# Kernel optimization log

Hardware: AMD Instinct MI355X
Metric: run time of the kernel (lower is better)

## Reference

```python
import jax, jax.numpy as jnp
import numpy as np

K_DIM, V_DIM, D_K, D_V, N_HEAD = 1024, 1024, 64, 64, 16


def setup_inputs() -> dict:
    key = jax.random.key(0)
    ks = jax.random.split(key, 7)
    B, LQ, LK = 2, 2048, 2048
    q = jax.random.normal(ks[0], (B, LQ, K_DIM), dtype=jnp.float32)
    k = jax.random.normal(ks[1], (B, LK, K_DIM), dtype=jnp.float32)
    v = jax.random.normal(ks[2], (B, LK, V_DIM), dtype=jnp.float32)
    s = 0.02
    w_q = jax.random.normal(ks[3], (N_HEAD * D_K, K_DIM), dtype=jnp.float32) * s
    w_k = jax.random.normal(ks[4], (N_HEAD * D_K, K_DIM), dtype=jnp.float32) * s
    w_v = jax.random.normal(ks[5], (N_HEAD * D_V, V_DIM), dtype=jnp.float32) * s
    fc_y = jax.random.normal(ks[6], (V_DIM, N_HEAD * D_V), dtype=jnp.float32) * s
    return {"q": q, "k": k, "v": v, "w_q": w_q, "w_k": w_k, "w_v": w_v, "fc_y": fc_y}


def reference(q, k, v, w_q, w_k, w_v, fc_y):
    B, LQ, _ = q.shape
    LK = k.shape[1]
    # projections: Linear(x) = x @ W.T, then split heads -> (b, h, l, d)
    qh = (q @ w_q.T).reshape(B, LQ, N_HEAD, D_K).transpose(0, 2, 1, 3)
    kh = (k @ w_k.T).reshape(B, LK, N_HEAD, D_K).transpose(0, 2, 1, 3)
    vh = (v @ w_v.T).reshape(B, LK, N_HEAD, D_V).transpose(0, 2, 1, 3)
    # NOTE: original ScaledDotProductAttention uses k.size(2), which for
    # 4D (b, h, len_k, d_k) inputs is len_k, NOT d_k. Replicate faithfully.
    scale = kh.shape[2] ** 0.5  # == sqrt(len_k)
    scores = jnp.einsum('bhqd,bhkd->bhqk', qh, kh) / scale
    attn = jax.nn.softmax(scores, axis=-1)  # (b, h, lq, lk)
    yh = jnp.einsum('bhqk,bhkd->bhqd', attn, vh)
    y = yh.transpose(0, 2, 1, 3).reshape(B, LQ, N_HEAD * D_V)
    y = y @ fc_y.T  # (b, lq, v_dim)
    return (y, attn)
```

## Files before the change

### kernel.cpp

```cpp
#include <hip/hip_runtime.h>

typedef __attribute__((ext_vector_type(8))) short short8;
typedef __attribute__((ext_vector_type(4))) short short4v;
typedef __attribute__((ext_vector_type(4))) float f32x4;

__device__ __forceinline__ short f2bf(float f) {
  unsigned u = __float_as_uint(f);
  u += 0x7fff + ((u >> 16) & 1);
  return (short)(u >> 16);
}

__device__ __forceinline__ void async16(const short* g, short* l) {
  __builtin_amdgcn_global_load_lds(
      (__attribute__((address_space(1))) unsigned int*)(g),
      (__attribute__((address_space(3))) unsigned int*)(l), 16, 0, 0);
}

__global__ __launch_bounds__(256) void cvt_w(const float* __restrict__ w0, const float* __restrict__ w1,
                                             const float* __restrict__ w2, const float* __restrict__ w3,
                                             short* __restrict__ o0, short* __restrict__ o1,
                                             short* __restrict__ o2, short* __restrict__ o3) {
  const int bid = blockIdx.x;
  const int seg = bid >> 9;
  const float* s = seg == 0 ? w0 : seg == 1 ? w1 : seg == 2 ? w2 : w3;
  short* d = seg == 0 ? o0 : seg == 1 ? o1 : seg == 2 ? o2 : o3;
  const int idx = ((bid & 511) * 256 + (int)threadIdx.x) * 8;
  float4 x = *(const float4*)(s + idx);
  float4 y = *(const float4*)(s + idx + 4);
  short8 t;
  t[0] = f2bf(x.x); t[1] = f2bf(x.y); t[2] = f2bf(x.z); t[3] = f2bf(x.w);
  t[4] = f2bf(y.x); t[5] = f2bf(y.y); t[6] = f2bf(y.z); t[7] = f2bf(y.w);
  *(short8*)(d + idx) = t;
}

__device__ __forceinline__ void ldf32(const float* src, int K, int kt, int tid, f32x4* r) {
  const int row = tid >> 4, c = (tid & 15) * 4;
  const float* p = src + (long)row * K + kt + c;
#pragma unroll
  for (int j = 0; j < 8; j++) r[j] = *(const f32x4*)(p + (long)(j * 16) * K);
}
__device__ __forceinline__ void wrf32(short* dst, int stride, int tid, const f32x4* r) {
  const int row = tid >> 4, c = (tid & 15) * 4;
#pragma unroll
  for (int j = 0; j < 8; j++) {
    short4v t;
    t[0] = f2bf(r[j][0]); t[1] = f2bf(r[j][1]); t[2] = f2bf(r[j][2]); t[3] = f2bf(r[j][3]);
    *(short4v*)&dst[(row + j * 16) * stride + c] = t;
  }
}
__device__ __forceinline__ void ldbf16(const short* src, int K, int kt, int tid, short* lds) {
  const int w = tid >> 6, l = tid & 63;
#pragma unroll
  for (int i = 0; i < 4; i++) {
    const int seg = i * 4 + w;
    const int o = seg * 1024 + l * 16;
    const int row = o >> 7, col = (o & 127) >> 1;
    async16(src + (long)row * K + kt + col, lds + seg * 512);
  }
}

template <int AF32, int BF32, int MODE>
__device__ __forceinline__ void gemm_core(const void* Ap, const void* Bp, void* Cout,
                                          int bm, int bn, int bz, int N, int K, int tid,
                                          short* As, short* Bs) {
  constexpr int SA = AF32 ? 72 : 64;
  constexpr int SB = BF32 ? 72 : 64;
  const int wave = tid >> 6, lane = tid & 63, quad = lane >> 4, l16 = lane & 15;
  const int wm = (wave >> 1) * 64, wn = (wave & 1) * 64;
  const float* A32 = (const float*)Ap + (long)bm * 128 * K;
  const short* A16 = (const short*)Ap + (long)bm * 128 * K;
  const float* B32 = (const float*)Bp + (long)bn * 128 * K;
  const short* B16 = (const short*)Bp + (long)bn * 128 * K;

  const f32x4 zero = {0.f, 0.f, 0.f, 0.f};
  f32x4 acc[4][4];
#pragma unroll
  for (int i = 0; i < 4; i++)
#pragma unroll
    for (int j = 0; j < 4; j++) acc[i][j] = zero;

  f32x4 ar[8], br[8];
  if (AF32) { ldf32(A32, K, 0, tid, ar); wrf32(As, SA, tid, ar); }
  else ldbf16(A16, K, 0, tid, As);
  if (BF32) { ldf32(B32, K, 0, tid, br); wrf32(Bs, SB, tid, br); }
  else ldbf16(B16, K, 0, tid, Bs);
  __syncthreads();

  const int NT = K >> 6;
  int cur = 0;
  for (int t = 0; t < NT; ++t) {
    short* Ac = As + cur * 128 * SA;
    short* Bc = Bs + cur * 128 * SB;
    short* An = As + (cur ^ 1) * 128 * SA;
    short* Bn = Bs + (cur ^ 1) * 128 * SB;
    const bool more = (t + 1 < NT);
    if (more) {
      if (AF32) ldf32(A32, K, (t + 1) * 64, tid, ar);
      else ldbf16(A16, K, (t + 1) * 64, tid, An);
      if (BF32) ldf32(B32, K, (t + 1) * 64, tid, br);
      else ldbf16(B16, K, (t + 1) * 64, tid, Bn);
    }
#pragma unroll
    for (int kk = 0; kk < 64; kk += 32) {
      short8 af[4], bf[4];
#pragma unroll
      for (int i = 0; i < 4; i++) af[i] = *(const short8*)&Ac[(wm + i * 16 + l16) * SA + kk + quad * 8];
#pragma unroll
      for (int j = 0; j < 4; j++) bf[j] = *(const short8*)&Bc[(wn + j * 16 + l16) * SB + kk + quad * 8];
#pragma unroll
      for (int i = 0; i < 4; i++)
#pragma unroll
        for (int j = 0; j < 4; j++)
          acc[i][j] = __builtin_amdgcn_mfma_f32_16x16x32_bf16(af[i], bf[j], acc[i][j], 0, 0, 0);
    }
    if (more) {
      if (AF32) wrf32(An, SA, tid, ar);
      if (BF32) wrf32(Bn, SB, tid, br);
    }
    __syncthreads();
    cur ^= 1;
  }

#pragma unroll
  for (int i = 0; i < 4; i++)
#pragma unroll
    for (int j = 0; j < 4; j++)
#pragma unroll
      for (int r = 0; r < 4; r++) {
        const int grow = bm * 128 + wm + i * 16 + quad * 4 + r;
        const int gcol = bn * 128 + wn + j * 16 + l16;
        const float val = acc[i][j][r];
        if (MODE == 0) {
          const int b = grow >> 11, l = grow & 2047, hh = gcol >> 6, d = gcol & 63;
          ((short*)Cout)[((long)(b * 16 + hh) * 2048 + l) * 64 + d] = f2bf(val);
        } else if (MODE == 1) {
          ((short*)Cout)[((long)bz * 1024 + grow) * 2048 + gcol] = f2bf(val);
        } else {
          ((float*)Cout)[(long)grow * N + gcol] = val;
        }
      }
}

__global__ __launch_bounds__(256) void proj_fused(const float* __restrict__ q, const float* __restrict__ k,
                                                  const float* __restrict__ v,
                                                  const short* __restrict__ wqb, const short* __restrict__ wkb,
                                                  const short* __restrict__ wvb,
                                                  short* __restrict__ qh, short* __restrict__ kh,
                                                  short* __restrict__ vht) {
  __shared__ __align__(16) short As[2 * 128 * 72];
  __shared__ __align__(16) short Bs[2 * 128 * 72];
  const int id = blockIdx.x, tid = threadIdx.x;
  if (id < 512) {
    const int seg = id >> 8, lid = id & 255;
    gemm_core<1, 0, 0>(seg ? (const void*)k : (const void*)q,
                       seg ? (const void*)wkb : (const void*)wqb,
                       seg ? (void*)kh : (void*)qh,
                       lid & 31, lid >> 5, 0, 1024, 1024, tid, As, Bs);
  } else {
    const int lid = id - 512;
    const int bz = lid >> 7;
    gemm_core<0, 1, 1>(wvb, v + (long)bz * 2048 * 1024, vht,
                       lid & 7, (lid >> 3) & 15, bz, 2048, 1024, tid, As, Bs);
  }
}

__global__ __launch_bounds__(256) void gemm_final(const short* __restrict__ yhb, const short* __restrict__ fcb,
                                                  float* __restrict__ y) {
  __shared__ __align__(16) short As[2 * 128 * 72];
  __shared__ __align__(16) short Bs[2 * 128 * 72];
  gemm_core<0, 0, 2>(yhb, fcb, y, blockIdx.x, blockIdx.y, 0, 1024, 1024, threadIdx.x, As, Bs);
}

__global__ __launch_bounds__(256) void attn_kernel(const short* __restrict__ qh, const short* __restrict__ kh,
                                                   const short* __restrict__ vht,
                                                   float* __restrict__ attn_out, short* __restrict__ yhb) {
  __shared__ __align__(16) short k_s[64][72];
  __shared__ __align__(16) short v_s[64][72];
  __shared__ __align__(16) short p_s[64][72];
  constexpr float SCALE = 0.022097086912079608f;

  const int qb = blockIdx.x, h = blockIdx.y, b = blockIdx.z;
  const long bh = b * 16 + h;
  const short* Q = qh + bh * (2048L * 64) + (long)qb * 64 * 64;
  const short* Kp = kh + bh * (2048L * 64);
  const short* Vt = vht + bh * (64L * 2048);
  float* attnp = attn_out + bh * (2048L * 2048) + (long)qb * 64 * 2048;

  const int tid = threadIdx.x;
  const int wave = tid >> 6, lane = tid & 63, quad = lane >> 4, l16 = lane & 15;
  const int myrow0 = wave * 16;
  const int srow = tid >> 2, sch = (tid & 3) * 16;
  const f32x4 zero = {0.f, 0.f, 0.f, 0.f};

  const short8 qa0 = *(const short8*)(Q + (myrow0 + l16) * 64 + quad * 8);
  const short8 qa1 = *(const short8*)(Q + (myrow0 + l16) * 64 + 32 + quad * 8);

  float lrow[4] = {0.f, 0.f, 0.f, 0.f};

  *(short8*)&k_s[srow][sch] = *(const short8*)(Kp + srow * 64 + sch);
  *(short8*)&k_s[srow][sch + 8] = *(const short8*)(Kp + srow * 64 + sch + 8);
  __syncthreads();
  for (int kt = 0; kt < 32; ++kt) {
    short(*cb)[72] = (kt & 1) ? v_s : k_s;
    short(*nb)[72] = (kt & 1) ? k_s : v_s;
    short8 n0, n1;
    if (kt < 31) {
      const short* Kn = Kp + ((kt + 1) * 64 + srow) * 64 + sch;
      n0 = *(const short8*)(Kn);
      n1 = *(const short8*)(Kn + 8);
    }
#pragma unroll
    for (int nt = 0; nt < 4; ++nt) {
      short8 b0 = *(const short8*)&cb[nt * 16 + l16][quad * 8];
      short8 b1 = *(const short8*)&cb[nt * 16 + l16][32 + quad * 8];
      f32x4 c = zero;
      c = __builtin_amdgcn_mfma_f32_16x16x32_bf16(qa0, b0, c, 0, 0, 0);
      c = __builtin_amdgcn_mfma_f32_16x16x32_bf16(qa1, b1, c, 0, 0, 0);
#pragma unroll
      for (int r = 0; r < 4; ++r) lrow[r] += __expf(c[r] * SCALE);
    }
    if (kt < 31) {
      *(short8*)&nb[srow][sch] = n0;
      *(short8*)&nb[srow][sch + 8] = n1;
    }
    __syncthreads();
  }
#pragma unroll
  for (int r = 0; r < 4; ++r) {
    float l = lrow[r];
#pragma unroll
    for (int off = 1; off < 16; off <<= 1) l += __shfl_xor(l, off);
    lrow[r] = 1.0f / l;
  }

  f32x4 oacc[4];
#pragma unroll
  for (int nt = 0; nt < 4; ++nt) oacc[nt] = zero;
  *(short8*)&k_s[srow][sch] = *(const short8*)(Kp + srow * 64 + sch);
  *(short8*)&k_s[srow][sch + 8] = *(const short8*)(Kp + srow * 64 + sch + 8);
  *(short8*)&v_s[srow][sch] = *(const short8*)(Vt + (long)srow * 2048 + sch);
  *(short8*)&v_s[srow][sch + 8] = *(const short8*)(Vt + (long)srow * 2048 + sch + 8);
  __syncthreads();
  for (int kt = 0; kt < 32; ++kt) {
    short8 nk0, nk1, nv0, nv1;
    if (kt < 31) {
      const short* Kn = Kp + ((kt + 1) * 64 + srow) * 64 + sch;
      nk0 = *(const short8*)(Kn);
      nk1 = *(const short8*)(Kn + 8);
      const short* Vn = Vt + (long)srow * 2048 + (kt + 1) * 64 + sch;
      nv0 = *(const short8*)(Vn);
      nv1 = *(const short8*)(Vn + 8);
    }
#pragma unroll
    for (int nt = 0; nt < 4; ++nt) {
      short8 b0 = *(const short8*)&k_s[nt * 16 + l16][quad * 8];
      short8 b1 = *(const short8*)&k_s[nt * 16 + l16][32 + quad * 8];
      f32x4 c = zero;
      c = __builtin_amdgcn_mfma_f32_16x16x32_bf16(qa0, b0, c, 0, 0, 0);
      c = __builtin_amdgcn_mfma_f32_16x16x32_bf16(qa1, b1, c, 0, 0, 0);
#pragma unroll
      for (int r = 0; r < 4; ++r) {
        const float p = __expf(c[r] * SCALE) * lrow[r];
        const int prow = myrow0 + quad * 4 + r;
        __builtin_nontemporal_store(p, &attnp[(long)prow * 2048 + kt * 64 + nt * 16 + l16]);
        p_s[prow][nt * 16 + l16] = f2bf(p);
      }
    }
    short8 pa0 = *(const short8*)&p_s[myrow0 + l16][quad * 8];
    short8 pa1 = *(const short8*)&p_s[myrow0 + l16][32 + quad * 8];
#pragma unroll
    for (int nt = 0; nt < 4; ++nt) {
      short8 vb0 = *(const short8*)&v_s[nt * 16 + l16][quad * 8];
      short8 vb1 = *(const short8*)&v_s[nt * 16 + l16][32 + quad * 8];
      oacc[nt] = __builtin_amdgcn_mfma_f32_16x16x32_bf16(pa0, vb0, oacc[nt], 0, 0, 0);
      oacc[nt] = __builtin_amdgcn_mfma_f32_16x16x32_bf16(pa1, vb1, oacc[nt], 0, 0, 0);
    }
    __syncthreads();
    if (kt < 31) {
      *(short8*)&k_s[srow][sch] = nk0;
      *(short8*)&k_s[srow][sch + 8] = nk1;
      *(short8*)&v_s[srow][sch] = nv0;
      *(short8*)&v_s[srow][sch + 8] = nv1;
    }
    __syncthreads();
  }

#pragma unroll
  for (int nt = 0; nt < 4; ++nt)
#pragma unroll
    for (int r = 0; r < 4; ++r) {
      const long l = (long)qb * 64 + myrow0 + quad * 4 + r;
      const int d = nt * 16 + l16;
      yhb[((long)b * 2048 + l) * 1024 + h * 64 + d] = f2bf(oacc[nt][r]);
    }
}

extern "C" void kernel_launch(void* const* d_in, const int* in_sizes, int n_in,
                              void* d_out, int out_size, void* d_ws, size_t ws_size,
                              hipStream_t stream) {
  const float* q = (const float*)d_in[0];
  const float* k = (const float*)d_in[1];
  const float* v = (const float*)d_in[2];
  const float* wq = (const float*)d_in[3];
  const float* wk = (const float*)d_in[4];
  const float* wv = (const float*)d_in[5];
  const float* fcy = (const float*)d_in[6];

  float* y_out = (float*)d_out;
  float* attn_out = (float*)d_out + 4194304;

  char* ws = (char*)d_ws;
  short* qh = (short*)(ws);
  short* kh = (short*)(ws + 8388608);
  short* vht = (short*)(ws + 16777216);
  short* yhb = (short*)(ws + 25165824);
  short* wqb = (short*)(ws + 33554432);
  short* wkb = (short*)(ws + 35651584);
  short* wvb = (short*)(ws + 37748736);
  short* fcb = (short*)(ws + 39845888);

  cvt_w<<<2048, 256, 0, stream>>>(wq, wk, wv, fcy, wqb, wkb, wvb, fcb);
  proj_fused<<<768, 256, 0, stream>>>(q, k, v, wqb, wkb, wvb, qh, kh, vht);
  attn_kernel<<<dim3(32, 16, 2), 256, 0, stream>>>(qh, kh, vht, attn_out, yhb);
  gemm_final<<<dim3(32, 8), 256, 0, stream>>>(yhb, fcb, y_out);
}
```

Before: 792.6 us.

## Reorder attention passes to normalize PV at the end, and remap GEMM block order

The attention kernel now runs the P·V accumulation pass first with unnormalized exponentials, summing row totals along the way, and scales the output by the reciprocal sum at the end. A second QK pass then recomputes the scores only to write the normalized attention matrix. This takes the PV MFMA work and V loads off the pass that stores the attention matrix, so the large nontemporal store stream can run on its own. The projection and final GEMMs also remap block indices so that consecutive blocks are spread across XCDs in groups of eight, aiming for better L2 locality. The total work stays about the same: two QK passes as before. Without max subtraction, unnormalized bf16 P values could differ slightly in rounding.

```diff
diff --git a/kernel.cpp b/kernel.cpp
--- a/kernel.cpp
+++ b/kernel.cpp
@@ -149,18 +149,20 @@
                                                   short* __restrict__ vht) {
   __shared__ __align__(16) short As[2 * 128 * 72];
   __shared__ __align__(16) short Bs[2 * 128 * 72];
-  const int id = blockIdx.x, tid = threadIdx.x;
+  const int p = blockIdx.x, tid = threadIdx.x;
+  const int id = (p & 7) * 96 + (p >> 3);
   if (id < 512) {
-    const int seg = id >> 8, lid = id & 255;
+    const int seg = id >> 8, t = id & 255;
+    const int bm = t >> 3, bn = t & 7;
     gemm_core<1, 0, 0>(seg ? (const void*)k : (const void*)q,
                        seg ? (const void*)wkb : (const void*)wqb,
                        seg ? (void*)kh : (void*)qh,
-                       lid & 31, lid >> 5, 0, 1024, 1024, tid, As, Bs);
+                       bm, bn, 0, 1024, 1024, tid, As, Bs);
   } else {
     const int lid = id - 512;
-    const int bz = lid >> 7;
+    const int bz = lid >> 7, t = lid & 127;
     gemm_core<0, 1, 1>(wvb, v + (long)bz * 2048 * 1024, vht,
-                       lid & 7, (lid >> 3) & 15, bz, 2048, 1024, tid, As, Bs);
+                       t & 7, t >> 3, bz, 2048, 1024, tid, As, Bs);
   }
 }
 
@@ -168,7 +170,9 @@
                                                   float* __restrict__ y) {
   __shared__ __align__(16) short As[2 * 128 * 72];
   __shared__ __align__(16) short Bs[2 * 128 * 72];
-  gemm_core<0, 0, 2>(yhb, fcb, y, blockIdx.x, blockIdx.y, 0, 1024, 1024, threadIdx.x, As, Bs);
+  const int p = blockIdx.x;
+  const int id = (p & 7) * 32 + (p >> 3);
+  gemm_core<0, 0, 2>(yhb, fcb, y, id >> 3, id & 7, 0, 1024, 1024, threadIdx.x, As, Bs);
 }
 
 __global__ __launch_bounds__(256) void attn_kernel(const short* __restrict__ qh, const short* __restrict__ kh,
@@ -196,46 +200,10 @@
   const short8 qa1 = *(const short8*)(Q + (myrow0 + l16) * 64 + 32 + quad * 8);
 
   float lrow[4] = {0.f, 0.f, 0.f, 0.f};
-
-  *(short8*)&k_s[srow][sch] = *(const short8*)(Kp + srow * 64 + sch);
-  *(short8*)&k_s[srow][sch + 8] = *(const short8*)(Kp + srow * 64 + sch + 8);
-  __syncthreads();
-  for (int kt = 0; kt < 32; ++kt) {
-    short(*cb)[72] = (kt & 1) ? v_s : k_s;
-    short(*nb)[72] = (kt & 1) ? k_s : v_s;
-    short8 n0, n1;
-    if (kt < 31) {
-      const short* Kn = Kp + ((kt + 1) * 64 + srow) * 64 + sch;
-      n0 = *(const short8*)(Kn);
-      n1 = *(const short8*)(Kn + 8);
-    }
-#pragma unroll
-    for (int nt = 0; nt < 4; ++nt) {
-      short8 b0 = *(const short8*)&cb[nt * 16 + l16][quad * 8];
-      short8 b1 = *(const short8*)&cb[nt * 16 + l16][32 + quad * 8];
-      f32x4 c = zero;
-      c = __builtin_amdgcn_mfma_f32_16x16x32_bf16(qa0, b0, c, 0, 0, 0);
-      c = __builtin_amdgcn_mfma_f32_16x16x32_bf16(qa1, b1, c, 0, 0, 0);
-#pragma unroll
-      for (int r = 0; r < 4; ++r) lrow[r] += __expf(c[r] * SCALE);
-    }
-    if (kt < 31) {
-      *(short8*)&nb[srow][sch] = n0;
-      *(short8*)&nb[srow][sch + 8] = n1;
-    }
-    __syncthreads();
-  }
-#pragma unroll
-  for (int r = 0; r < 4; ++r) {
-    float l = lrow[r];
-#pragma unroll
-    for (int off = 1; off < 16; off <<= 1) l += __shfl_xor(l, off);
-    lrow[r] = 1.0f / l;
-  }
-
   f32x4 oacc[4];
 #pragma unroll
   for (int nt = 0; nt < 4; ++nt) oacc[nt] = zero;
+
   *(short8*)&k_s[srow][sch] = *(const short8*)(Kp + srow * 64 + sch);
   *(short8*)&k_s[srow][sch + 8] = *(const short8*)(Kp + srow * 64 + sch + 8);
   *(short8*)&v_s[srow][sch] = *(const short8*)(Vt + (long)srow * 2048 + sch);
@@ -260,10 +228,9 @@
       c = __builtin_amdgcn_mfma_f32_16x16x32_bf16(qa1, b1, c, 0, 0, 0);
 #pragma unroll
       for (int r = 0; r < 4; ++r) {
-        const float p = __expf(c[r] * SCALE) * lrow[r];
-        const int prow = myrow0 + quad * 4 + r;
-        __builtin_nontemporal_store(p, &attnp[(long)prow * 2048 + kt * 64 + nt * 16 + l16]);
-        p_s[prow][nt * 16 + l16] = f2bf(p);
+        const float p = __expf(c[r] * SCALE);
+        lrow[r] += p;
+        p_s[myrow0 + quad * 4 + r][nt * 16 + l16] = f2bf(p);
       }
     }
     short8 pa0 = *(const short8*)&p_s[myrow0 + l16][quad * 8];
@@ -285,14 +252,56 @@
     __syncthreads();
   }
 
+  float rinv[4];
+#pragma unroll
+  for (int r = 0; r < 4; ++r) {
+    float l = lrow[r];
+#pragma unroll
+    for (int off = 1; off < 16; off <<= 1) l += __shfl_xor(l, off);
+    rinv[r] = 1.0f / l;
+  }
+
 #pragma unroll
   for (int nt = 0; nt < 4; ++nt)
 #pragma unroll
     for (int r = 0; r < 4; ++r) {
       const long l = (long)qb * 64 + myrow0 + quad * 4 + r;
       const int d = nt * 16 + l16;
-      yhb[((long)b * 2048 + l) * 1024 + h * 64 + d] = f2bf(oacc[nt][r]);
-    }
+      yhb[((long)b * 2048 + l) * 1024 + h * 64 + d] = f2bf(oacc[nt][r] * rinv[r]);
+    }
+
+  *(short8*)&k_s[srow][sch] = *(const short8*)(Kp + srow * 64 + sch);
+  *(short8*)&k_s[srow][sch + 8] = *(const short8*)(Kp + srow * 64 + sch + 8);
+  __syncthreads();
+  for (int kt = 0; kt < 32; ++kt) {
+    short(*cb)[72] = (kt & 1) ? v_s : k_s;
+    short(*nb)[72] = (kt & 1) ? k_s : v_s;
+    short8 n0, n1;
+    if (kt < 31) {
+      const short* Kn = Kp + ((kt + 1) * 64 + srow) * 64 + sch;
+      n0 = *(const short8*)(Kn);
+      n1 = *(const short8*)(Kn + 8);
+    }
+#pragma unroll
+    for (int nt = 0; nt < 4; ++nt) {
+      short8 b0 = *(const short8*)&cb[nt * 16 + l16][quad * 8];
+      short8 b1 = *(const short8*)&cb[nt * 16 + l16][32 + quad * 8];
+      f32x4 c = zero;
+      c = __builtin_amdgcn_mfma_f32_16x16x32_bf16(qa0, b0, c, 0, 0, 0);
+      c = __builtin_amdgcn_mfma_f32_16x16x32_bf16(qa1, b1, c, 0, 0, 0);
+#pragma unroll
+      for (int r = 0; r < 4; ++r) {
+        const float pv = __expf(c[r] * SCALE) * rinv[r];
+        __builtin_nontemporal_store(
+            pv, &attnp[(long)(myrow0 + quad * 4 + r) * 2048 + kt * 64 + nt * 16 + l16]);
+      }
+    }
+    if (kt < 31) {
+      *(short8*)&nb[srow][sch] = n0;
+      *(short8*)&nb[srow][sch + 8] = n1;
+    }
+    __syncthreads();
+  }
 }
 
 extern "C" void kernel_launch(void* const* d_in, const int* in_sizes, int n_in,
@@ -322,5 +331,5 @@
   cvt_w<<<2048, 256, 0, stream>>>(wq, wk, wv, fcy, wqb, wkb, wvb, fcb);
   proj_fused<<<768, 256, 0, stream>>>(q, k, v, wqb, wkb, wvb, qh, kh, vht);
   attn_kernel<<<dim3(32, 16, 2), 256, 0, stream>>>(qh, kh, vht, attn_out, yhb);
-  gemm_final<<<dim3(32, 8), 256, 0, stream>>>(yhb, fcb, y_out);
-}
+  gemm_final<<<dim3(256), 256, 0, stream>>>(yhb, fcb, y_out);
+}
```

New measurement: 799.8 us. About the same (+0.9%).
